# Optimization experiments

Measured on AMD Instinct MI355X. Metric: run time of the kernel, lower is better.

## Reference

```python
import jax, jax.numpy as jnp
import numpy as np

N_NODES = 50000
N_EDGES = 800000
D_IN, D_HID, N_CLS, N_PROT = 128, 256, 16, 512
EPS = 1e-6


def setup_inputs() -> dict:
    key = jax.random.key(0)
    ks = jax.random.split(key, 12)
    s = 0.05
    return {
        "x": jax.random.normal(ks[0], (N_NODES, D_IN), dtype=jnp.float32),
        "edge_index": jax.random.randint(ks[1], (2, N_EDGES), 0, N_NODES, dtype=jnp.int64),
        "prot": jax.random.randint(ks[2], (N_PROT,), 0, N_NODES, dtype=jnp.int64),
        "epoch": 1,
        "W0": jax.random.normal(ks[3], (D_IN, D_HID), dtype=jnp.float32) * s,
        "b0": jnp.zeros((D_HID,), jnp.float32),
        "W1": jax.random.normal(ks[4], (D_HID, D_HID), dtype=jnp.float32) * s,
        "b1": jnp.zeros((D_HID,), jnp.float32),
        "Wl1": jax.random.normal(ks[5], (D_HID, D_HID), dtype=jnp.float32) * s,
        "bl1": jnp.zeros((D_HID,), jnp.float32),
        "Wl2": jax.random.normal(ks[6], (D_HID, N_CLS), dtype=jnp.float32) * s,
        "bl2": jnp.zeros((N_CLS,), jnp.float32),
    }


def _gcn_layer(h, W, b, src, dst, norm, n):
    # PyG GCNConv: h' = scatter_add(norm * (h @ W)[src] -> dst) + b
    m = (h @ W)[src] * norm[:, None]
    return jax.ops.segment_sum(m, dst, num_segments=n) + b


def _forward(x, edge_index, prot, W0, b0, W1, b1, Wl1, bl1, Wl2, bl2):
    n = x.shape[0]
    loops = jnp.arange(n, dtype=edge_index.dtype)
    src = jnp.concatenate([edge_index[0], loops])
    dst = jnp.concatenate([edge_index[1], loops])
    deg = jax.ops.segment_sum(jnp.ones_like(dst, dtype=x.dtype), dst, num_segments=n)
    dis = jax.lax.rsqrt(deg)  # deg >= 1 thanks to self loops
    norm = dis[src] * dis[dst]

    h = jax.nn.relu(_gcn_layer(x, W0, b0, src, dst, norm, n))
    h = _gcn_layer(h, W1, b1, src, dst, norm, n)

    # L2 row-normalize (torch divides by the norm directly)
    qn = jnp.linalg.norm(h, axis=1, keepdims=True)
    h = h / qn

    # relative_rep: cosine similarity of every node to each anchor
    anchors = h[prot]                             # [P, H]
    nx = jnp.linalg.norm(h, axis=1)               # [N]
    na = jnp.linalg.norm(anchors, axis=1)         # [P]
    num = h @ anchors.T                           # [N, P]
    x_rel = num / jnp.maximum(nx[:, None] * na[None, :], EPS)

    # classifier head on prototypes -> out_proto, then composed prediction
    lin = lambda z: jax.nn.relu(z @ Wl1 + bl1) @ Wl2 + bl2
    out_proto = jax.nn.log_softmax(lin(anchors), axis=-1)   # [P, C]
    out = jax.nn.log_softmax(x_rel @ out_proto, axis=-1)    # [N, C]
    return out, x_rel, out_proto


def reference(x, edge_index, prot, epoch, W0, b0, W1, b1, Wl1, bl1, Wl2, bl2):
    # epoch >= first_step_epochs (=0) branch: inference-path composition
    return _forward(x, edge_index, prot, W0, b0, W1, b1, Wl1, bl1, Wl2, bl2)


if __name__ == "__main__":
    out, x_rel, out_proto = reference(**setup_inputs())
    print(out.shape, x_rel.shape, out_proto.shape)
```

## Files before the change

kernel.cpp:

```cpp
#include <hip/hip_runtime.h>
#include <hip/hip_bf16.h>
#include <math.h>

#define NN 50000
#define NP 50048
#define EE 800000
#define DIN 128
#define HID 256
#define NCLS 16
#define NPROT 512

typedef __attribute__((ext_vector_type(8))) short short8;
typedef __attribute__((ext_vector_type(4))) float f32x4;

__device__ inline unsigned short f2b(float f) {
    union { float f; unsigned u; } c; c.f = f;
    unsigned u = c.u;
    unsigned r = (u + 0x7FFFu + ((u >> 16) & 1u)) >> 16;
    return (unsigned short)r;
}
__device__ inline float b2f(unsigned short u) {
    union { unsigned u; float f; } c; c.u = ((unsigned)u) << 16; return c.f;
}

#define GL2LDS16(g, l)                                                              \
    __builtin_amdgcn_global_load_lds(                                               \
        (const __attribute__((address_space(1))) unsigned int*)(g),                 \
        (__attribute__((address_space(3))) unsigned int*)(l), 16, 0, 0)


__global__ __launch_bounds__(256) void k_count(const int* __restrict__ dst, int* __restrict__ cnt, int e) {
    int i = blockIdx.x * 256 + threadIdx.x;
    if (i < e) atomicAdd(&cnt[dst[i]], 1);
}

__global__ __launch_bounds__(256) void k_dis(const int* __restrict__ cnt, float* __restrict__ dis, int n) {
    int i = blockIdx.x * 256 + threadIdx.x;
    if (i < n) dis[i] = rsqrtf((float)cnt[i] + 1.0f);
}

__global__ __launch_bounds__(256) void k_scan1(const int* __restrict__ cnt, int* __restrict__ excl,
                                               int* __restrict__ bsum, int n) {
    __shared__ int s[256];
    int t = threadIdx.x;
    int i = blockIdx.x * 256 + t;
    int v = (i < n) ? cnt[i] : 0;
    s[t] = v; __syncthreads();
    for (int d = 1; d < 256; d <<= 1) {
        int add = (t >= d) ? s[t - d] : 0;
        __syncthreads();
        s[t] += add;
        __syncthreads();
    }
    if (i < n) excl[i] = s[t] - v;
    if (t == 255) bsum[blockIdx.x] = s[255];
}

__global__ __launch_bounds__(256) void k_scan2(const int* __restrict__ bsum, int* __restrict__ boff, int nb) {
    __shared__ int s[256];
    int t = threadIdx.x;
    int v = (t < nb) ? bsum[t] : 0;
    s[t] = v; __syncthreads();
    for (int d = 1; d < 256; d <<= 1) {
        int add = (t >= d) ? s[t - d] : 0;
        __syncthreads();
        s[t] += add;
        __syncthreads();
    }
    if (t < nb) boff[t] = s[t] - v;
}

__global__ __launch_bounds__(256) void k_scan3(const int* __restrict__ excl, const int* __restrict__ boff,
                                               int* __restrict__ off, int n, int e) {
    int i = blockIdx.x * 256 + threadIdx.x;
    if (i < n) off[i] = excl[i] + boff[blockIdx.x];
    if (i == 0) off[n] = e;
}

__global__ __launch_bounds__(256) void k_fill(const int* __restrict__ src, const int* __restrict__ dst,
                                              const int* __restrict__ off, int* __restrict__ cursor,
                                              const float* __restrict__ dis,
                                              int* __restrict__ csr_src, float* __restrict__ csr_norm, int e) {
    int i = blockIdx.x * 256 + threadIdx.x;
    if (i >= e) return;
    int s = src[i], d = dst[i];
    int pos = atomicAdd(&cursor[d], 1);
    int slot = off[d] + pos;
    csr_src[slot] = s;
    csr_norm[slot] = dis[s] * dis[d];
}


__global__ __launch_bounds__(256) void k_cast(const float* __restrict__ x, unsigned short* __restrict__ xb, int n4) {
    int i = blockIdx.x * 256 + threadIdx.x;
    if (i >= n4) return;
    float4 v = ((const float4*)x)[i];
    ushort4 o; o.x = f2b(v.x); o.y = f2b(v.y); o.z = f2b(v.z); o.w = f2b(v.w);
    ((ushort4*)xb)[i] = o;
}

__global__ __launch_bounds__(256) void k_wt(const float* __restrict__ W, unsigned short* __restrict__ Wt,
                                            int K, int Nn) {
    int i = blockIdx.x * 256 + threadIdx.x;
    if (i >= K * Nn) return;
    int k = i / Nn, n = i - k * Nn;
    Wt[n * K + k] = f2b(W[(size_t)k * Nn + n]);
}


__global__ __launch_bounds__(256) void k_gemm_mfma(const unsigned short* __restrict__ A,
                                                   const unsigned short* __restrict__ Bt,
                                                   void* __restrict__ C, int M, int Nc, int K, int mode,
                                                   const float* __restrict__ nx, const float* __restrict__ na) {
    __shared__ __align__(16) unsigned short As[128 * 32];
    __shared__ __align__(16) unsigned short Bs[128 * 32];
    const int t = threadIdx.x;
    const int lane = t & 63;
    const int quad = lane >> 4;
    const int l16 = lane & 15;
    const int wv = t >> 6;
    const int wm = (wv & 1) * 64, wn = (wv >> 1) * 64;
    const int m0 = blockIdx.y * 128, n0 = blockIdx.x * 128;

    f32x4 acc[4][4];
#pragma unroll
    for (int i = 0; i < 4; ++i)
#pragma unroll
        for (int j = 0; j < 4; ++j)
#pragma unroll
            for (int r = 0; r < 4; ++r) acc[i][j][r] = 0.0f;

    const int sr = t >> 2;
    const int sc = (t & 3) * 8;

    for (int k0 = 0; k0 < K; k0 += 32) {
        GL2LDS16(A + (size_t)(m0 + sr) * K + k0 + sc,       &As[t * 8]);
        GL2LDS16(A + (size_t)(m0 + 64 + sr) * K + k0 + sc,  &As[2048 + t * 8]);
        GL2LDS16(Bt + (size_t)(n0 + sr) * K + k0 + sc,      &Bs[t * 8]);
        GL2LDS16(Bt + (size_t)(n0 + 64 + sr) * K + k0 + sc, &Bs[2048 + t * 8]);
        __syncthreads();
        short8 af[4], bf[4];
#pragma unroll
        for (int i = 0; i < 4; ++i)
            af[i] = *(const short8*)&As[(wm + i * 16 + l16) * 32 + quad * 8];
#pragma unroll
        for (int j = 0; j < 4; ++j)
            bf[j] = *(const short8*)&Bs[(wn + j * 16 + l16) * 32 + quad * 8];
#pragma unroll
        for (int i = 0; i < 4; ++i)
#pragma unroll
            for (int j = 0; j < 4; ++j)
                acc[i][j] = __builtin_amdgcn_mfma_f32_16x16x32_bf16(af[i], bf[j], acc[i][j], 0, 0, 0);
        __syncthreads();
    }

#pragma unroll
    for (int i = 0; i < 4; ++i) {
        int rb = m0 + wm + i * 16 + quad * 4;
#pragma unroll
        for (int j = 0; j < 4; ++j) {
            int col = n0 + wn + j * 16 + l16;
#pragma unroll
            for (int rg = 0; rg < 4; ++rg) {
                int r = rb + rg;
                float v = acc[i][j][rg];
                if (mode == 0) {
                    ((unsigned short*)C)[(size_t)r * Nc + col] = f2b(v);
                } else if (r < M) {
                    float s = fmaxf(nx[r] * na[col], 1e-6f);
                    ((float*)C)[(size_t)r * Nc + col] = v / s;
                }
            }
        }
    }
}


__global__ __launch_bounds__(256) void k_agg(const unsigned short* __restrict__ xw, const int* __restrict__ off,
                                             const int* __restrict__ esrc, const float* __restrict__ enorm,
                                             const float* __restrict__ dis, const float* __restrict__ bias,
                                             unsigned short* __restrict__ out, float* __restrict__ nx,
                                             int n, int mode) {
    int node = (blockIdx.x * 256 + threadIdx.x) >> 6;
    int lane = threadIdx.x & 63;
    if (node >= n) return;
    float d = dis[node];
    float w0 = d * d;
    ushort4 u = ((const ushort4*)(xw + (size_t)node * HID))[lane];
    float a0 = w0 * b2f(u.x), a1 = w0 * b2f(u.y), a2 = w0 * b2f(u.z), a3 = w0 * b2f(u.w);
    int p = off[node], p1 = off[node + 1];
    for (; p + 1 < p1; p += 2) {
        int s0 = esrc[p], s1 = esrc[p + 1];
        float w_0 = enorm[p], w_1 = enorm[p + 1];
        ushort4 v0 = ((const ushort4*)(xw + (size_t)s0 * HID))[lane];
        ushort4 v1 = ((const ushort4*)(xw + (size_t)s1 * HID))[lane];
        a0 = fmaf(w_0, b2f(v0.x), a0); a1 = fmaf(w_0, b2f(v0.y), a1);
        a2 = fmaf(w_0, b2f(v0.z), a2); a3 = fmaf(w_0, b2f(v0.w), a3);
        a0 = fmaf(w_1, b2f(v1.x), a0); a1 = fmaf(w_1, b2f(v1.y), a1);
        a2 = fmaf(w_1, b2f(v1.z), a2); a3 = fmaf(w_1, b2f(v1.w), a3);
    }
    if (p < p1) {
        int s0 = esrc[p];
        float w_0 = enorm[p];
        ushort4 v0 = ((const ushort4*)(xw + (size_t)s0 * HID))[lane];
        a0 = fmaf(w_0, b2f(v0.x), a0); a1 = fmaf(w_0, b2f(v0.y), a1);
        a2 = fmaf(w_0, b2f(v0.z), a2); a3 = fmaf(w_0, b2f(v0.w), a3);
    }
    float4 b = ((const float4*)bias)[lane];
    a0 += b.x; a1 += b.y; a2 += b.z; a3 += b.w;
    if (mode == 1) {
        a0 = fmaxf(a0, 0.f); a1 = fmaxf(a1, 0.f); a2 = fmaxf(a2, 0.f); a3 = fmaxf(a3, 0.f);
    } else {
        float ss = a0 * a0 + a1 * a1 + a2 * a2 + a3 * a3;
        for (int m = 32; m >= 1; m >>= 1) ss += __shfl_xor(ss, m, 64);
        float qn = sqrtf(ss);
        a0 /= qn; a1 /= qn; a2 /= qn; a3 /= qn;
        float s2 = a0 * a0 + a1 * a1 + a2 * a2 + a3 * a3;
        for (int m = 32; m >= 1; m >>= 1) s2 += __shfl_xor(s2, m, 64);
        if (lane == 0) nx[node] = sqrtf(s2);
    }
    ushort4 o; o.x = f2b(a0); o.y = f2b(a1); o.z = f2b(a2); o.w = f2b(a3);
    ((ushort4*)(out + (size_t)node * HID))[lane] = o;
}


__global__ __launch_bounds__(256) void k_gather(const unsigned short* __restrict__ hb, const int* __restrict__ prot,
                                                const float* __restrict__ nx,
                                                float* __restrict__ aR, unsigned short* __restrict__ aRb,
                                                float* __restrict__ na, int p_cnt) {
    int a = (blockIdx.x * 256 + threadIdx.x) >> 6;
    int lane = threadIdx.x & 63;
    if (a >= p_cnt) return;
    int p = prot[a];
    ushort4 v = ((const ushort4*)(hb + (size_t)p * HID))[lane];
    ((ushort4*)(aRb + (size_t)a * HID))[lane] = v;
    float4 f; f.x = b2f(v.x); f.y = b2f(v.y); f.z = b2f(v.z); f.w = b2f(v.w);
    *reinterpret_cast<float4*>(aR + (size_t)a * HID + lane * 4) = f;
    if (lane == 0) na[a] = nx[p];
}


__global__ __launch_bounds__(256) void k_proto(const float* __restrict__ aR, const float* __restrict__ Wl1,
                                               const float* __restrict__ bl1, const float* __restrict__ Wl2,
                                               const float* __restrict__ bl2, float* __restrict__ outp) {
    __shared__ float sa[HID];
    __shared__ float st[HID];
    int row = blockIdx.x, t = threadIdx.x;
    sa[t] = aR[(size_t)row * HID + t];
    __syncthreads();
    float acc = bl1[t];
#pragma unroll 8
    for (int k = 0; k < HID; ++k) acc = fmaf(sa[k], Wl1[k * HID + t], acc);
    st[t] = fmaxf(acc, 0.0f);
    __syncthreads();
    if (t < 64) {
        int c = t & 15, ch = t >> 4;
        float z = 0.f;
#pragma unroll 8
        for (int k = ch * 64; k < ch * 64 + 64; ++k) z = fmaf(st[k], Wl2[k * NCLS + c], z);
        z += __shfl_xor(z, 16, 64);
        z += __shfl_xor(z, 32, 64);
        z += bl2[c];
        float m = z;
        for (int d = 8; d >= 1; d >>= 1) m = fmaxf(m, __shfl_xor(m, d, 64));
        float e = expf(z - m);
        float s = e;
        for (int d = 8; d >= 1; d >>= 1) s += __shfl_xor(s, d, 64);
        if (t < 16) outp[row * NCLS + c] = z - m - logf(s);
    }
}


__global__ __launch_bounds__(256) void k_final(const float* __restrict__ xrel, const float* __restrict__ proto,
                                               float* __restrict__ out, int M) {
    __shared__ __align__(16) unsigned short pT[16 * 520];
    int t = threadIdx.x;
    for (int i = t; i < NPROT * NCLS; i += 256) {
        int k = i >> 4, c = i & 15;
        pT[c * 520 + k] = f2b(proto[i]);
    }
    __syncthreads();
    const int lane = t & 63, wv = t >> 6;
    const int quad = lane >> 4, l16 = lane & 15;
    short8 bfr[16];
#pragma unroll
    for (int ks = 0; ks < 16; ++ks)
        bfr[ks] = *(const short8*)&pT[l16 * 520 + ks * 32 + quad * 8];
    int m0 = blockIdx.x * 128;
#pragma unroll
    for (int mt = 0; mt < 2; ++mt) {
        int tile0 = m0 + (wv * 2 + mt) * 16;
        int r = tile0 + l16;
        int rl = (r < M) ? r : (M - 1);
        const float* xr = xrel + (size_t)rl * NPROT + quad * 8;
        f32x4 acc = {0.f, 0.f, 0.f, 0.f};
#pragma unroll
        for (int ks = 0; ks < 16; ++ks) {
            float4 v0 = *(const float4*)(xr + ks * 32);
            float4 v1 = *(const float4*)(xr + ks * 32 + 4);
            short8 af;
            af[0] = (short)f2b(v0.x); af[1] = (short)f2b(v0.y);
            af[2] = (short)f2b(v0.z); af[3] = (short)f2b(v0.w);
            af[4] = (short)f2b(v1.x); af[5] = (short)f2b(v1.y);
            af[6] = (short)f2b(v1.z); af[7] = (short)f2b(v1.w);
            acc = __builtin_amdgcn_mfma_f32_16x16x32_bf16(af, bfr[ks], acc, 0, 0, 0);
        }
#pragma unroll
        for (int rg = 0; rg < 4; ++rg) {
            int row = tile0 + quad * 4 + rg;
            float z = acc[rg];
            float mx = z;
            for (int d = 8; d >= 1; d >>= 1) mx = fmaxf(mx, __shfl_xor(mx, d, 64));
            float e = expf(z - mx);
            float s = e;
            for (int d = 8; d >= 1; d >>= 1) s += __shfl_xor(s, d, 64);
            if (row < M) out[(size_t)row * NCLS + l16] = z - mx - logf(s);
        }
    }
}


extern "C" void kernel_launch(void* const* d_in, const int* in_sizes, int n_in,
                              void* d_out, int out_size, void* d_ws, size_t ws_size,
                              hipStream_t stream) {
    const float* x    = (const float*)d_in[0];
    const int*   eidx = (const int*)d_in[1];
    const int*   prot = (const int*)d_in[2];
    const float* W0  = (const float*)d_in[4];
    const float* b0  = (const float*)d_in[5];
    const float* W1  = (const float*)d_in[6];
    const float* b1  = (const float*)d_in[7];
    const float* Wl1 = (const float*)d_in[8];
    const float* bl1 = (const float*)d_in[9];
    const float* Wl2 = (const float*)d_in[10];
    const float* bl2 = (const float*)d_in[11];

    const int N = NN, E = EE;
    const int* esrc_in = eidx;
    const int* edst_in = eidx + E;

    float* out_final = (float*)d_out;
    float* x_rel     = (float*)d_out + (size_t)N * NCLS;
    float* out_proto = x_rel + (size_t)N * NPROT;

    char* w = (char*)d_ws;
    auto alloc = [&](size_t bytes) { char* p = w; w += (bytes + 255) & ~(size_t)255; return p; };
    int*   cnt      = (int*)alloc((size_t)N * 4);
    int*   cursor   = (int*)alloc((size_t)N * 4);
    float* dis      = (float*)alloc((size_t)N * 4);
    int*   excl     = (int*)alloc((size_t)N * 4);
    int*   csr_off  = (int*)alloc((size_t)(N + 1) * 4);
    int*   bsum     = (int*)alloc(1024);
    int*   boff     = (int*)alloc(1024);
    int*   csr_src  = (int*)alloc((size_t)E * 4);
    float* csr_norm = (float*)alloc((size_t)E * 4);
    float* nx       = (float*)alloc((size_t)N * 4);
    float* na       = (float*)alloc((size_t)NPROT * 4);
    unsigned short* xb    = (unsigned short*)alloc((size_t)NP * DIN * 2);
    unsigned short* Wt0   = (unsigned short*)alloc((size_t)HID * DIN * 2);
    unsigned short* Wt1   = (unsigned short*)alloc((size_t)HID * HID * 2);
    unsigned short* bufAb = (unsigned short*)alloc((size_t)NP * HID * 2);
    unsigned short* h0b   = (unsigned short*)alloc((size_t)NP * HID * 2);
    float* aR       = (float*)alloc((size_t)NPROT * HID * 4);
    unsigned short* aRb   = (unsigned short*)alloc((size_t)NPROT * HID * 2);
    unsigned short* hb = h0b;

    hipMemsetAsync(cnt, 0, (size_t)N * 4, stream);
    hipMemsetAsync(cursor, 0, (size_t)N * 4, stream);

    k_count<<<(E + 255) / 256, 256, 0, stream>>>(edst_in, cnt, E);
    k_dis<<<(N + 255) / 256, 256, 0, stream>>>(cnt, dis, N);
    int NB = (N + 255) / 256;
    k_scan1<<<NB, 256, 0, stream>>>(cnt, excl, bsum, N);
    k_scan2<<<1, 256, 0, stream>>>(bsum, boff, NB);
    k_scan3<<<NB, 256, 0, stream>>>(excl, boff, csr_off, N, E);
    k_fill<<<(E + 255) / 256, 256, 0, stream>>>(esrc_in, edst_in, csr_off, cursor, dis, csr_src, csr_norm, E);

    k_cast<<<(N * DIN / 4 + 255) / 256, 256, 0, stream>>>(x, xb, N * DIN / 4);
    k_wt<<<(DIN * HID + 255) / 256, 256, 0, stream>>>(W0, Wt0, DIN, HID);
    k_wt<<<(HID * HID + 255) / 256, 256, 0, stream>>>(W1, Wt1, HID, HID);

    const int MT = NP / 128;

    k_gemm_mfma<<<dim3(HID / 128, MT), 256, 0, stream>>>(xb, Wt0, bufAb, N, HID, DIN, 0, nullptr, nullptr);
    k_agg<<<N / 4, 256, 0, stream>>>(bufAb, csr_off, csr_src, csr_norm, dis, b0, h0b, nullptr, N, 1);

    k_gemm_mfma<<<dim3(HID / 128, MT), 256, 0, stream>>>(h0b, Wt1, bufAb, N, HID, HID, 0, nullptr, nullptr);
    k_agg<<<N / 4, 256, 0, stream>>>(bufAb, csr_off, csr_src, csr_norm, dis, b1, hb, nx, N, 2);

    k_gather<<<NPROT / 4, 256, 0, stream>>>(hb, prot, nx, aR, aRb, na, NPROT);

    k_gemm_mfma<<<dim3(NPROT / 128, MT), 256, 0, stream>>>(hb, aRb, x_rel, N, NPROT, HID, 1, nx, na);

    k_proto<<<NPROT, 256, 0, stream>>>(aR, Wl1, bl1, Wl2, bl2, out_proto);
    k_final<<<MT, 256, 0, stream>>>(x_rel, out_proto, out_final, N);
}
```

Baseline: 530.3 us.

## Aggregate before first GEMM, pack CSR edges, fuse small prep kernels

```diff
diff --git a/kernel.cpp b/kernel.cpp
--- a/kernel.cpp
+++ b/kernel.cpp
@@ -34,17 +34,13 @@
     if (i < e) atomicAdd(&cnt[dst[i]], 1);
 }
 
-__global__ __launch_bounds__(256) void k_dis(const int* __restrict__ cnt, float* __restrict__ dis, int n) {
-    int i = blockIdx.x * 256 + threadIdx.x;
-    if (i < n) dis[i] = rsqrtf((float)cnt[i] + 1.0f);
-}
-
 __global__ __launch_bounds__(256) void k_scan1(const int* __restrict__ cnt, int* __restrict__ excl,
-                                               int* __restrict__ bsum, int n) {
+                                               int* __restrict__ bsum, float* __restrict__ dis, int n) {
     __shared__ int s[256];
     int t = threadIdx.x;
     int i = blockIdx.x * 256 + t;
     int v = (i < n) ? cnt[i] : 0;
+    if (i < n) dis[i] = rsqrtf((float)v + 1.0f);
     s[t] = v; __syncthreads();
     for (int d = 1; d < 256; d <<= 1) {
         int add = (t >= d) ? s[t - d] : 0;
@@ -80,38 +76,45 @@
 __global__ __launch_bounds__(256) void k_fill(const int* __restrict__ src, const int* __restrict__ dst,
                                               const int* __restrict__ off, int* __restrict__ cursor,
                                               const float* __restrict__ dis,
-                                              int* __restrict__ csr_src, float* __restrict__ csr_norm, int e) {
+                                              int2* __restrict__ csr_e, int e) {
     int i = blockIdx.x * 256 + threadIdx.x;
     if (i >= e) return;
     int s = src[i], d = dst[i];
     int pos = atomicAdd(&cursor[d], 1);
-    int slot = off[d] + pos;
-    csr_src[slot] = s;
-    csr_norm[slot] = dis[s] * dis[d];
-}
-
-
-__global__ __launch_bounds__(256) void k_cast(const float* __restrict__ x, unsigned short* __restrict__ xb, int n4) {
-    int i = blockIdx.x * 256 + threadIdx.x;
-    if (i >= n4) return;
-    float4 v = ((const float4*)x)[i];
-    ushort4 o; o.x = f2b(v.x); o.y = f2b(v.y); o.z = f2b(v.z); o.w = f2b(v.w);
-    ((ushort4*)xb)[i] = o;
-}
-
-__global__ __launch_bounds__(256) void k_wt(const float* __restrict__ W, unsigned short* __restrict__ Wt,
-                                            int K, int Nn) {
-    int i = blockIdx.x * 256 + threadIdx.x;
-    if (i >= K * Nn) return;
-    int k = i / Nn, n = i - k * Nn;
-    Wt[n * K + k] = f2b(W[(size_t)k * Nn + n]);
+    csr_e[off[d] + pos] = make_int2(s, __float_as_int(dis[s] * dis[d]));
+}
+
+
+#define CAST_BLKS (NN * DIN / 4 / 256)
+#define WT0_BLKS  (DIN * HID / 256)
+#define WT1_BLKS  (HID * HID / 256)
+
+__global__ __launch_bounds__(256) void k_prep(const float* __restrict__ x, unsigned short* __restrict__ xb,
+                                              const float* __restrict__ W0, unsigned short* __restrict__ Wt0,
+                                              const float* __restrict__ W1, unsigned short* __restrict__ Wt1) {
+    int b = blockIdx.x, t = threadIdx.x;
+    if (b < CAST_BLKS) {
+        int i = b * 256 + t;
+        float4 v = ((const float4*)x)[i];
+        ushort4 o; o.x = f2b(v.x); o.y = f2b(v.y); o.z = f2b(v.z); o.w = f2b(v.w);
+        ((ushort4*)xb)[i] = o;
+    } else if (b < CAST_BLKS + WT0_BLKS) {
+        int i = (b - CAST_BLKS) * 256 + t;
+        int k = i / HID, n = i - k * HID;
+        Wt0[n * DIN + k] = f2b(W0[(size_t)k * HID + n]);
+    } else {
+        int i = (b - CAST_BLKS - WT0_BLKS) * 256 + t;
+        int k = i / HID, n = i - k * HID;
+        Wt1[n * HID + k] = f2b(W1[(size_t)k * HID + n]);
+    }
 }
 
 
 __global__ __launch_bounds__(256) void k_gemm_mfma(const unsigned short* __restrict__ A,
                                                    const unsigned short* __restrict__ Bt,
                                                    void* __restrict__ C, int M, int Nc, int K, int mode,
-                                                   const float* __restrict__ nx, const float* __restrict__ na) {
+                                                   const float* __restrict__ nx, const float* __restrict__ na,
+                                                   const float* __restrict__ bias) {
     __shared__ __align__(16) unsigned short As[128 * 32];
     __shared__ __align__(16) unsigned short Bs[128 * 32];
     const int t = threadIdx.x;
@@ -166,6 +169,9 @@
                 float v = acc[i][j][rg];
                 if (mode == 0) {
                     ((unsigned short*)C)[(size_t)r * Nc + col] = f2b(v);
+                } else if (mode == 2) {
+                    v = fmaxf(v + bias[col], 0.0f);
+                    ((unsigned short*)C)[(size_t)r * Nc + col] = f2b(v);
                 } else if (r < M) {
                     float s = fmaxf(nx[r] * na[col], 1e-6f);
                     ((float*)C)[(size_t)r * Nc + col] = v / s;
@@ -176,11 +182,38 @@
 }
 
 
-__global__ __launch_bounds__(256) void k_agg(const unsigned short* __restrict__ xw, const int* __restrict__ off,
-                                             const int* __restrict__ esrc, const float* __restrict__ enorm,
-                                             const float* __restrict__ dis, const float* __restrict__ bias,
-                                             unsigned short* __restrict__ out, float* __restrict__ nx,
-                                             int n, int mode) {
+__global__ __launch_bounds__(256) void k_agg128(const unsigned short* __restrict__ xw, const int* __restrict__ off,
+                                                const int2* __restrict__ csr, const float* __restrict__ dis,
+                                                unsigned short* __restrict__ out, int n) {
+    int node = (blockIdx.x * 256 + threadIdx.x) >> 6;
+    int lane = threadIdx.x & 63;
+    if (node >= n) return;
+    float d = dis[node];
+    float w0 = d * d;
+    ushort2 u = ((const ushort2*)(xw + (size_t)node * DIN))[lane];
+    float a0 = w0 * b2f(u.x), a1 = w0 * b2f(u.y);
+    int p = off[node], p1 = off[node + 1];
+#define G128(e)                                                           \
+    {                                                                     \
+        ushort2 v = ((const ushort2*)(xw + (size_t)(e).x * DIN))[lane];   \
+        float w = __int_as_float((e).y);                                  \
+        a0 = fmaf(w, b2f(v.x), a0); a1 = fmaf(w, b2f(v.y), a1);           \
+    }
+    for (; p + 3 < p1; p += 4) {
+        int2 e0 = csr[p], e1 = csr[p + 1], e2 = csr[p + 2], e3 = csr[p + 3];
+        G128(e0) G128(e1) G128(e2) G128(e3)
+    }
+    for (; p < p1; ++p) { int2 e0 = csr[p]; G128(e0) }
+#undef G128
+    ushort2 o; o.x = f2b(a0); o.y = f2b(a1);
+    ((ushort2*)(out + (size_t)node * DIN))[lane] = o;
+}
+
+
+__global__ __launch_bounds__(256) void k_agg256(const unsigned short* __restrict__ xw, const int* __restrict__ off,
+                                                const int2* __restrict__ csr, const float* __restrict__ dis,
+                                                const float* __restrict__ bias,
+                                                unsigned short* __restrict__ out, float* __restrict__ nx, int n) {
     int node = (blockIdx.x * 256 + threadIdx.x) >> 6;
     int lane = threadIdx.x & 63;
     if (node >= n) return;
@@ -189,64 +222,47 @@
     ushort4 u = ((const ushort4*)(xw + (size_t)node * HID))[lane];
     float a0 = w0 * b2f(u.x), a1 = w0 * b2f(u.y), a2 = w0 * b2f(u.z), a3 = w0 * b2f(u.w);
     int p = off[node], p1 = off[node + 1];
-    for (; p + 1 < p1; p += 2) {
-        int s0 = esrc[p], s1 = esrc[p + 1];
-        float w_0 = enorm[p], w_1 = enorm[p + 1];
-        ushort4 v0 = ((const ushort4*)(xw + (size_t)s0 * HID))[lane];
-        ushort4 v1 = ((const ushort4*)(xw + (size_t)s1 * HID))[lane];
-        a0 = fmaf(w_0, b2f(v0.x), a0); a1 = fmaf(w_0, b2f(v0.y), a1);
-        a2 = fmaf(w_0, b2f(v0.z), a2); a3 = fmaf(w_0, b2f(v0.w), a3);
-        a0 = fmaf(w_1, b2f(v1.x), a0); a1 = fmaf(w_1, b2f(v1.y), a1);
-        a2 = fmaf(w_1, b2f(v1.z), a2); a3 = fmaf(w_1, b2f(v1.w), a3);
-    }
-    if (p < p1) {
-        int s0 = esrc[p];
-        float w_0 = enorm[p];
-        ushort4 v0 = ((const ushort4*)(xw + (size_t)s0 * HID))[lane];
-        a0 = fmaf(w_0, b2f(v0.x), a0); a1 = fmaf(w_0, b2f(v0.y), a1);
-        a2 = fmaf(w_0, b2f(v0.z), a2); a3 = fmaf(w_0, b2f(v0.w), a3);
-    }
+#define G256(e)                                                           \
+    {                                                                     \
+        ushort4 v = ((const ushort4*)(xw + (size_t)(e).x * HID))[lane];   \
+        float w = __int_as_float((e).y);                                  \
+        a0 = fmaf(w, b2f(v.x), a0); a1 = fmaf(w, b2f(v.y), a1);           \
+        a2 = fmaf(w, b2f(v.z), a2); a3 = fmaf(w, b2f(v.w), a3);           \
+    }
+    for (; p + 3 < p1; p += 4) {
+        int2 e0 = csr[p], e1 = csr[p + 1], e2 = csr[p + 2], e3 = csr[p + 3];
+        G256(e0) G256(e1) G256(e2) G256(e3)
+    }
+    for (; p < p1; ++p) { int2 e0 = csr[p]; G256(e0) }
+#undef G256
     float4 b = ((const float4*)bias)[lane];
     a0 += b.x; a1 += b.y; a2 += b.z; a3 += b.w;
-    if (mode == 1) {
-        a0 = fmaxf(a0, 0.f); a1 = fmaxf(a1, 0.f); a2 = fmaxf(a2, 0.f); a3 = fmaxf(a3, 0.f);
-    } else {
-        float ss = a0 * a0 + a1 * a1 + a2 * a2 + a3 * a3;
-        for (int m = 32; m >= 1; m >>= 1) ss += __shfl_xor(ss, m, 64);
-        float qn = sqrtf(ss);
-        a0 /= qn; a1 /= qn; a2 /= qn; a3 /= qn;
-        float s2 = a0 * a0 + a1 * a1 + a2 * a2 + a3 * a3;
-        for (int m = 32; m >= 1; m >>= 1) s2 += __shfl_xor(s2, m, 64);
-        if (lane == 0) nx[node] = sqrtf(s2);
-    }
+    float ss = a0 * a0 + a1 * a1 + a2 * a2 + a3 * a3;
+    for (int m = 32; m >= 1; m >>= 1) ss += __shfl_xor(ss, m, 64);
+    float qn = sqrtf(ss);
+    a0 /= qn; a1 /= qn; a2 /= qn; a3 /= qn;
+    float s2 = a0 * a0 + a1 * a1 + a2 * a2 + a3 * a3;
+    for (int m = 32; m >= 1; m >>= 1) s2 += __shfl_xor(s2, m, 64);
+    if (lane == 0) nx[node] = sqrtf(s2);
     ushort4 o; o.x = f2b(a0); o.y = f2b(a1); o.z = f2b(a2); o.w = f2b(a3);
     ((ushort4*)(out + (size_t)node * HID))[lane] = o;
 }
 
 
-__global__ __launch_bounds__(256) void k_gather(const unsigned short* __restrict__ hb, const int* __restrict__ prot,
-                                                const float* __restrict__ nx,
-                                                float* __restrict__ aR, unsigned short* __restrict__ aRb,
-                                                float* __restrict__ na, int p_cnt) {
-    int a = (blockIdx.x * 256 + threadIdx.x) >> 6;
-    int lane = threadIdx.x & 63;
-    if (a >= p_cnt) return;
-    int p = prot[a];
-    ushort4 v = ((const ushort4*)(hb + (size_t)p * HID))[lane];
-    ((ushort4*)(aRb + (size_t)a * HID))[lane] = v;
-    float4 f; f.x = b2f(v.x); f.y = b2f(v.y); f.z = b2f(v.z); f.w = b2f(v.w);
-    *reinterpret_cast<float4*>(aR + (size_t)a * HID + lane * 4) = f;
-    if (lane == 0) na[a] = nx[p];
-}
-
-
-__global__ __launch_bounds__(256) void k_proto(const float* __restrict__ aR, const float* __restrict__ Wl1,
-                                               const float* __restrict__ bl1, const float* __restrict__ Wl2,
-                                               const float* __restrict__ bl2, float* __restrict__ outp) {
+__global__ __launch_bounds__(256) void k_gproto(const unsigned short* __restrict__ hb,
+                                                const int* __restrict__ prot, const float* __restrict__ nx,
+                                                unsigned short* __restrict__ aRb, float* __restrict__ na,
+                                                const float* __restrict__ Wl1, const float* __restrict__ bl1,
+                                                const float* __restrict__ Wl2, const float* __restrict__ bl2,
+                                                float* __restrict__ outp) {
     __shared__ float sa[HID];
     __shared__ float st[HID];
     int row = blockIdx.x, t = threadIdx.x;
-    sa[t] = aR[(size_t)row * HID + t];
+    int p = prot[row];
+    unsigned short us = hb[(size_t)p * HID + t];
+    aRb[(size_t)row * HID + t] = us;
+    sa[t] = b2f(us);
+    if (t == 0) na[row] = nx[p];
     __syncthreads();
     float acc = bl1[t];
 #pragma unroll 8
@@ -352,8 +368,7 @@
     int*   csr_off  = (int*)alloc((size_t)(N + 1) * 4);
     int*   bsum     = (int*)alloc(1024);
     int*   boff     = (int*)alloc(1024);
-    int*   csr_src  = (int*)alloc((size_t)E * 4);
-    float* csr_norm = (float*)alloc((size_t)E * 4);
+    int2*  csr_e    = (int2*)alloc((size_t)E * 8);
     float* nx       = (float*)alloc((size_t)N * 4);
     float* na       = (float*)alloc((size_t)NPROT * 4);
     unsigned short* xb    = (unsigned short*)alloc((size_t)NP * DIN * 2);
@@ -361,37 +376,33 @@
     unsigned short* Wt1   = (unsigned short*)alloc((size_t)HID * HID * 2);
     unsigned short* bufAb = (unsigned short*)alloc((size_t)NP * HID * 2);
     unsigned short* h0b   = (unsigned short*)alloc((size_t)NP * HID * 2);
-    float* aR       = (float*)alloc((size_t)NPROT * HID * 4);
     unsigned short* aRb   = (unsigned short*)alloc((size_t)NPROT * HID * 2);
+    unsigned short* a1 = bufAb;
     unsigned short* hb = h0b;
 
     hipMemsetAsync(cnt, 0, (size_t)N * 4, stream);
     hipMemsetAsync(cursor, 0, (size_t)N * 4, stream);
 
     k_count<<<(E + 255) / 256, 256, 0, stream>>>(edst_in, cnt, E);
-    k_dis<<<(N + 255) / 256, 256, 0, stream>>>(cnt, dis, N);
     int NB = (N + 255) / 256;
-    k_scan1<<<NB, 256, 0, stream>>>(cnt, excl, bsum, N);
+    k_scan1<<<NB, 256, 0, stream>>>(cnt, excl, bsum, dis, N);
     k_scan2<<<1, 256, 0, stream>>>(bsum, boff, NB);
     k_scan3<<<NB, 256, 0, stream>>>(excl, boff, csr_off, N, E);
-    k_fill<<<(E + 255) / 256, 256, 0, stream>>>(esrc_in, edst_in, csr_off, cursor, dis, csr_src, csr_norm, E);
-
-    k_cast<<<(N * DIN / 4 + 255) / 256, 256, 0, stream>>>(x, xb, N * DIN / 4);
-    k_wt<<<(DIN * HID + 255) / 256, 256, 0, stream>>>(W0, Wt0, DIN, HID);
-    k_wt<<<(HID * HID + 255) / 256, 256, 0, stream>>>(W1, Wt1, HID, HID);
+    k_fill<<<(E + 255) / 256, 256, 0, stream>>>(esrc_in, edst_in, csr_off, cursor, dis, csr_e, E);
+
+    k_prep<<<CAST_BLKS + WT0_BLKS + WT1_BLKS, 256, 0, stream>>>(x, xb, W0, Wt0, W1, Wt1);
 
     const int MT = NP / 128;
 
-    k_gemm_mfma<<<dim3(HID / 128, MT), 256, 0, stream>>>(xb, Wt0, bufAb, N, HID, DIN, 0, nullptr, nullptr);
-    k_agg<<<N / 4, 256, 0, stream>>>(bufAb, csr_off, csr_src, csr_norm, dis, b0, h0b, nullptr, N, 1);
-
-    k_gemm_mfma<<<dim3(HID / 128, MT), 256, 0, stream>>>(h0b, Wt1, bufAb, N, HID, HID, 0, nullptr, nullptr);
-    k_agg<<<N / 4, 256, 0, stream>>>(bufAb, csr_off, csr_src, csr_norm, dis, b1, hb, nx, N, 2);
-
-    k_gather<<<NPROT / 4, 256, 0, stream>>>(hb, prot, nx, aR, aRb, na, NPROT);
-
-    k_gemm_mfma<<<dim3(NPROT / 128, MT), 256, 0, stream>>>(hb, aRb, x_rel, N, NPROT, HID, 1, nx, na);
-
-    k_proto<<<NPROT, 256, 0, stream>>>(aR, Wl1, bl1, Wl2, bl2, out_proto);
+    k_agg128<<<(N + 3) / 4, 256, 0, stream>>>(xb, csr_off, csr_e, dis, a1, N);
+    k_gemm_mfma<<<dim3(HID / 128, MT), 256, 0, stream>>>(a1, Wt0, h0b, N, HID, DIN, 2, nullptr, nullptr, b0);
+
+    k_gemm_mfma<<<dim3(HID / 128, MT), 256, 0, stream>>>(h0b, Wt1, bufAb, N, HID, HID, 0, nullptr, nullptr, nullptr);
+    k_agg256<<<(N + 3) / 4, 256, 0, stream>>>(bufAb, csr_off, csr_e, dis, b1, hb, nx, N);
+
+    k_gproto<<<NPROT, 256, 0, stream>>>(hb, prot, nx, aRb, na, Wl1, bl1, Wl2, bl2, out_proto);
+
+    k_gemm_mfma<<<dim3(NPROT / 128, MT), 256, 0, stream>>>(hb, aRb, x_rel, N, NPROT, HID, 1, nx, na, nullptr);
+
     k_final<<<MT, 256, 0, stream>>>(x_rel, out_proto, out_final, N);
 }
```

Result: faster. 489.5 us (-7.7%).
